# Kernel tuning notes

Hardware: AMD Instinct MI355X
Metric: run time of the kernel (lower is better)

The kernel has to match this reference:

```python
import jax, jax.numpy as jnp
import numpy as np

D = 512
B, S = 4, 4096


def setup_inputs() -> dict:
    key = jax.random.key(0)
    ks = jax.random.split(key, 8)
    scale = 1.0 / np.sqrt(D)
    return {
        "x": jax.random.normal(ks[0], (B, S, D), dtype=jnp.float32),
        "bias": jax.random.normal(ks[1], (1, S, S), dtype=jnp.float32),
        "Wq_w": jax.random.normal(ks[2], (D, D), dtype=jnp.float32) * scale,
        "Wq_b": jax.random.normal(ks[3], (D,), dtype=jnp.float32) * 0.02,
        "Wk_w": jax.random.normal(ks[4], (D, D), dtype=jnp.float32) * scale,
        "Wk_b": jax.random.normal(ks[5], (D,), dtype=jnp.float32) * 0.02,
        "Wv_w": jax.random.normal(ks[6], (D, D), dtype=jnp.float32) * scale,
        "Wv_b": jax.random.normal(ks[7], (D,), dtype=jnp.float32) * 0.02,
    }


def reference(x, bias, Wq_w, Wq_b, Wk_w, Wk_b, Wv_w, Wv_b):
    # torch nn.Linear: y = x @ W.T + b
    q = jnp.einsum("bsd,ed->bse", x, Wq_w) + Wq_b
    k = jnp.einsum("bsd,ed->bse", x, Wk_w) + Wk_b
    v = jnp.einsum("bsd,ed->bse", x, Wv_w) + Wv_b
    inv_sqrt_d = jnp.asarray(1.0 / np.sqrt(D), dtype=x.dtype)
    # scores: [B, S, S] -- scale by sqrt(feature_dim) as in the original
    scores = jnp.einsum("bqd,bkd->bqk", q * inv_sqrt_d, k) + bias
    weights = jax.nn.sigmoid(scores)
    out = jnp.einsum("bqk,bkd->bqd", weights, v)
    return out
```

## Files before the change

### kernel.cpp

```cpp
#include <hip/hip_runtime.h>
#include <hip/hip_bf16.h>
#include <stdint.h>

typedef unsigned short bf16_t;
typedef __attribute__((ext_vector_type(4))) short s4v;
typedef __attribute__((ext_vector_type(8))) short short8;
typedef __attribute__((ext_vector_type(4))) float f32x4;

__device__ __forceinline__ bf16_t f2b(float f) {
    union { float f; uint32_t u; } v; v.f = f;
    uint32_t u = v.u;
    return (bf16_t)((u + 0x7FFFu + ((u >> 16) & 1u)) >> 16);
}

__global__ __launch_bounds__(256) void cvt_all(const float* __restrict__ x,
                                               bf16_t* __restrict__ Xb,
                                               const float* __restrict__ a,
                                               const float* __restrict__ b,
                                               const float* __restrict__ c,
                                               bf16_t* __restrict__ Wb) {
    int i = blockIdx.x * 256 + threadIdx.x;
    if (i < 2097152) {
        float4 f = ((const float4*)x)[i];
        ushort4 o;
        o.x = f2b(f.x); o.y = f2b(f.y); o.z = f2b(f.z); o.w = f2b(f.w);
        ((ushort4*)Xb)[i] = o;
    } else {
        int j = i - 2097152;
        const int which = j >> 16;
        const int idx   = j & 65535;
        const float* src = (which == 0) ? a : (which == 1) ? b : c;
        float4 f = ((const float4*)src)[idx];
        ushort4 o;
        o.x = f2b(f.x); o.y = f2b(f.y); o.z = f2b(f.z); o.w = f2b(f.w);
        ((ushort4*)Wb)[j] = o;
    }
}

__device__ __forceinline__ void lds_dma16(const void* g, void* l) {
    __builtin_amdgcn_global_load_lds(
        (const __attribute__((address_space(1))) void*)g,
        (__attribute__((address_space(3))) void*)l, 16, 0, 0);
}


__global__ __launch_bounds__(256)
void proj_all(const bf16_t* __restrict__ Xb, const bf16_t* __restrict__ Wb,
              const float* __restrict__ qb, const float* __restrict__ kb,
              const float* __restrict__ vb,
              bf16_t* __restrict__ Qb, bf16_t* __restrict__ Kb,
              bf16_t* __restrict__ Vt)
{
    __shared__ __align__(16) bf16_t lds[2][16384];

    const int tid  = threadIdx.x;
    const int bid  = blockIdx.x;
    const int lane = tid & 63;
    const int w    = tid >> 6;
    const int wm   = w & 1, wn = w >> 1;
    const int ll   = lane & 15;
    const int quad = lane >> 4;

    const int x     = bid & 7;
    const int g     = bid >> 3;
    const int mi    = x * 16 + g / 12;
    const int inner = g % 12;
    const int m0 = mi * 128;
    const int n0 = (inner & 3) * 128;
    const int z  = inner >> 2;

    const bf16_t* A = Xb;
    const bf16_t* B = Wb + z * 262144;

    auto stage = [&](int kt, int b) {
#pragma unroll
        for (int c = 0; c < 4; ++c) {
            const int base = (c * 4 + w) * 64;
            const int slot = base + lane;
            const int row  = slot >> 3;
            const int kc   = ((slot & 7) ^ (row & 7)) << 3;
            lds_dma16(A + (size_t)(m0 + row) * 512 + kt * 64 + kc, (char*)&lds[b][0]    + base * 16);
            lds_dma16(B + (size_t)(n0 + row) * 512 + kt * 64 + kc, (char*)&lds[b][8192] + base * 16);
        }
    };

    f32x4 acc[4][4];
#pragma unroll
    for (int i = 0; i < 4; i++)
#pragma unroll
        for (int j = 0; j < 4; j++) acc[i][j] = (f32x4){0.f, 0.f, 0.f, 0.f};

    stage(0, 0);
    __syncthreads();
    int cur = 0;
    for (int kt = 0; kt < 8; ++kt) {
        if (kt < 7) stage(kt + 1, cur ^ 1);
        const bf16_t* lsA = &lds[cur][0];
        const bf16_t* lsB = &lds[cur][8192];
#pragma unroll
        for (int t = 0; t < 2; t++) {
            short8 af[4], bf[4];
#pragma unroll
            for (int i = 0; i < 4; i++) {
                const int ri = wm * 64 + i * 16 + ll;
                const int rj = wn * 64 + i * 16 + ll;
                af[i] = *(const short8*)(lsA + ri * 64 + (((t * 4 + quad) ^ (ll & 7)) << 3));
                bf[i] = *(const short8*)(lsB + rj * 64 + (((t * 4 + quad) ^ (ll & 7)) << 3));
            }
#pragma unroll
            for (int i = 0; i < 4; i++)
#pragma unroll
                for (int j = 0; j < 4; j++)
                    acc[i][j] = __builtin_amdgcn_mfma_f32_16x16x32_bf16(af[i], bf[j], acc[i][j], 0, 0, 0);
        }
        __syncthreads();
        cur ^= 1;
    }

    bf16_t* wbuf = &lds[0][0] + w * 4096;
    const float inv = 0.044194173824159216f;

    if (z != 2) {
        const float* bptr = (z == 0) ? qb : kb;
        const float scl   = (z == 0) ? inv : 1.0f;
#pragma unroll
        for (int j = 0; j < 4; j++) {
            const int colL = j * 16 + ll;
            const float bv = bptr[n0 + wn * 64 + colL];
#pragma unroll
            for (int i = 0; i < 4; i++) {
                f32x4 a = acc[i][j];
#pragma unroll
                for (int r = 0; r < 4; r++) {
                    const int rowL = i * 16 + quad * 4 + r;
                    wbuf[rowL * 64 + (colL ^ ((rowL & 7) << 3))] = f2b((a[r] + bv) * scl);
                }
            }
        }
        __syncthreads();
        bf16_t* dst = (z == 0) ? Qb : Kb;
        const int rowg0 = m0 + wm * 64;
        const int colg0 = n0 + wn * 64;
#pragma unroll
        for (int k = 0; k < 8; k++) {
            const int rowL = (lane >> 3) + k * 8;
            const int c0   = (lane & 7) * 8;
            short8 vv = *(const short8*)(wbuf + rowL * 64 + (c0 ^ ((rowL & 7) << 3)));
            *(short8*)(dst + (size_t)(rowg0 + rowL) * 512 + colg0 + c0) = vv;
        }
    } else {
#pragma unroll
        for (int j = 0; j < 4; j++) {
            const int d = j * 16 + ll;
            const float bv = vb[n0 + wn * 64 + d];
#pragma unroll
            for (int i = 0; i < 4; i++) {
                f32x4 a = acc[i][j];
                s4v pk;
                pk[0] = (short)f2b(a[0] + bv);
                pk[1] = (short)f2b(a[1] + bv);
                pk[2] = (short)f2b(a[2] + bv);
                pk[3] = (short)f2b(a[3] + bv);
                const int sB = i * 16 + quad * 4;
                *(s4v*)(wbuf + d * 64 + (sB ^ ((d & 7) << 3))) = pk;
            }
        }
        __syncthreads();
        const int rowg0 = m0 + wm * 64;
        const int b  = rowg0 >> 12;
        const int s0 = rowg0 & 4095;
        const int d0 = n0 + wn * 64;
#pragma unroll
        for (int k = 0; k < 8; k++) {
            const int dL = (lane >> 3) + k * 8;
            const int c0 = (lane & 7) * 8;
            short8 vv = *(const short8*)(wbuf + dL * 64 + (c0 ^ ((dL & 7) << 3)));
            *(short8*)(Vt + ((size_t)b * 512 + d0 + dL) * 4096 + s0 + c0) = vv;
        }
    }
}

__global__ __launch_bounds__(256)
void scores_sig(const bf16_t* __restrict__ Qb, const bf16_t* __restrict__ Kb,
                const float* __restrict__ bias, bf16_t* __restrict__ P)
{
    __shared__ __align__(16) bf16_t lds[2][16384];

    const int tid  = threadIdx.x;
    const int lane = tid & 63;
    const int w    = tid >> 6;
    const int wm   = w & 1, wn = w >> 1;
    const int ll   = lane & 15;
    const int quad = lane >> 4;

    const int bx  = blockIdx.x;
    const int x   = bx & 7;
    const int s   = bx >> 3;
    const int z   = s & 3;
    const int t_  = x * 128 + (s >> 2);
    const int sup = t_ >> 5;
    const int win = t_ & 31;
    const int m0  = ((sup >> 2) * 4 + (win & 3)) * 128;
    const int n0  = ((sup & 3) * 8 + (win >> 2)) * 128;

    const bf16_t* A = Qb + (size_t)z * 2097152;
    const bf16_t* B = Kb + (size_t)z * 2097152;
    bf16_t* out = P + (size_t)z * 16777216;

    auto stage = [&](int kt, int b) {
#pragma unroll
        for (int c = 0; c < 4; ++c) {
            const int base = (c * 4 + w) * 64;
            const int slot = base + lane;
            const int row  = slot >> 3;
            const int kc   = ((slot & 7) ^ (row & 7)) << 3;
            lds_dma16(A + (size_t)(m0 + row) * 512 + kt * 64 + kc, (char*)&lds[b][0]    + base * 16);
            lds_dma16(B + (size_t)(n0 + row) * 512 + kt * 64 + kc, (char*)&lds[b][8192] + base * 16);
        }
    };

    f32x4 acc[4][4];
#pragma unroll
    for (int i = 0; i < 4; i++)
#pragma unroll
        for (int j = 0; j < 4; j++) acc[i][j] = (f32x4){0.f, 0.f, 0.f, 0.f};

    stage(0, 0);
    __syncthreads();
    int cur = 0;
    for (int kt = 0; kt < 8; ++kt) {
        if (kt < 7) stage(kt + 1, cur ^ 1);
        const bf16_t* lsA = &lds[cur][0];
        const bf16_t* lsB = &lds[cur][8192];
#pragma unroll
        for (int t = 0; t < 2; t++) {
            short8 af[4], bf[4];
#pragma unroll
            for (int i = 0; i < 4; i++) {
                const int ri = wm * 64 + i * 16 + ll;
                const int rj = wn * 64 + i * 16 + ll;
                af[i] = *(const short8*)(lsA + ri * 64 + (((t * 4 + quad) ^ (ll & 7)) << 3));
                bf[i] = *(const short8*)(lsB + rj * 64 + (((t * 4 + quad) ^ (ll & 7)) << 3));
            }
#pragma unroll
            for (int i = 0; i < 4; i++)
#pragma unroll
                for (int j = 0; j < 4; j++)
                    acc[i][j] = __builtin_amdgcn_mfma_f32_16x16x32_bf16(af[i], bf[j], acc[i][j], 0, 0, 0);
        }
        __syncthreads();
        cur ^= 1;
    }

#pragma unroll
    for (int i = 0; i < 4; i++) {
#pragma unroll
        for (int j = 0; j < 4; j++) {
            const int col  = n0 + wn * 64 + j * 16 + ll;
            const int rowb = m0 + wm * 64 + i * 16 + quad * 4;
            f32x4 a = acc[i][j];
#pragma unroll
            for (int r = 0; r < 4; r++) {
                const int row = rowb + r;
                const float v = a[r] + bias[(size_t)row * 4096 + col];
                const float p = __builtin_amdgcn_rcpf(1.f + __expf(-v));
                out[(size_t)row * 4096 + col] = (bf16_t)(__float_as_uint(p) >> 16);
            }
        }
    }
}

__global__ __launch_bounds__(256)
void pv_gemm(const bf16_t* __restrict__ P, const bf16_t* __restrict__ Vt,
             float* __restrict__ outg)
{
    __shared__ __align__(16) bf16_t lds[2][16384];

    const int tid  = threadIdx.x;
    const int lane = tid & 63;
    const int w    = tid >> 6;
    const int wm   = w & 1, wn = w >> 1;
    const int ll   = lane & 15;
    const int quad = lane >> 4;

    const int bid   = blockIdx.x;
    const int x     = bid & 7;
    const int g     = bid >> 3;
    const int strip = x * 16 + (g >> 2);
    const int n0    = (g & 3) * 128;
    const int m0    = (strip & 31) * 128;
    const int z     = strip >> 5;

    const bf16_t* A = P + (size_t)z * 16777216;
    const bf16_t* B = Vt + (size_t)z * 2097152;
    float* out = outg + (size_t)z * 2097152;

    auto stage = [&](int kt, int b) {
#pragma unroll
        for (int c = 0; c < 4; ++c) {
            const int base = (c * 4 + w) * 64;
            const int slot = base + lane;
            const int row  = slot >> 3;
            const int kc   = ((slot & 7) ^ (row & 7)) << 3;
            lds_dma16(A + (size_t)(m0 + row) * 4096 + kt * 64 + kc, (char*)&lds[b][0]    + base * 16);
            lds_dma16(B + (size_t)(n0 + row) * 4096 + kt * 64 + kc, (char*)&lds[b][8192] + base * 16);
        }
    };

    f32x4 acc[4][4];
#pragma unroll
    for (int i = 0; i < 4; i++)
#pragma unroll
        for (int j = 0; j < 4; j++) acc[i][j] = (f32x4){0.f, 0.f, 0.f, 0.f};

    stage(0, 0);
    __syncthreads();
    int cur = 0;
    for (int kt = 0; kt < 64; ++kt) {
        if (kt < 63) stage(kt + 1, cur ^ 1);
        const bf16_t* lsA = &lds[cur][0];
        const bf16_t* lsB = &lds[cur][8192];
#pragma unroll
        for (int t = 0; t < 2; t++) {
            short8 af[4], bf[4];
#pragma unroll
            for (int i = 0; i < 4; i++) {
                const int ri = wm * 64 + i * 16 + ll;
                const int rj = wn * 64 + i * 16 + ll;
                af[i] = *(const short8*)(lsA + ri * 64 + (((t * 4 + quad) ^ (ll & 7)) << 3));
                bf[i] = *(const short8*)(lsB + rj * 64 + (((t * 4 + quad) ^ (ll & 7)) << 3));
            }
#pragma unroll
            for (int i = 0; i < 4; i++)
#pragma unroll
                for (int j = 0; j < 4; j++)
                    acc[i][j] = __builtin_amdgcn_mfma_f32_16x16x32_bf16(af[i], bf[j], acc[i][j], 0, 0, 0);
        }
        __syncthreads();
        cur ^= 1;
    }

#pragma unroll
    for (int i = 0; i < 4; i++) {
#pragma unroll
        for (int j = 0; j < 4; j++) {
            const int col  = n0 + wn * 64 + j * 16 + ll;
            const int rowb = m0 + wm * 64 + i * 16 + quad * 4;
            f32x4 a = acc[i][j];
#pragma unroll
            for (int r = 0; r < 4; r++)
                out[(size_t)(rowb + r) * 512 + col] = a[r];
        }
    }
}

extern "C" void kernel_launch(void* const* d_in, const int* in_sizes, int n_in,
                              void* d_out, int out_size, void* d_ws, size_t ws_size,
                              hipStream_t stream) {
    (void)in_sizes; (void)n_in; (void)out_size; (void)ws_size;
    const float* x    = (const float*)d_in[0];
    const float* bias = (const float*)d_in[1];
    const float* Wq_w = (const float*)d_in[2];
    const float* Wq_b = (const float*)d_in[3];
    const float* Wk_w = (const float*)d_in[4];
    const float* Wk_b = (const float*)d_in[5];
    const float* Wv_w = (const float*)d_in[6];
    const float* Wv_b = (const float*)d_in[7];
    float* out = (float*)d_out;

    bf16_t* Xb = (bf16_t*)d_ws;
    bf16_t* Wb = Xb + (size_t)16384 * 512;
    bf16_t* Qb = Wb + (size_t)3 * 512 * 512;
    bf16_t* Kb = Qb + (size_t)16384 * 512;
    bf16_t* Vt = Kb + (size_t)16384 * 512;
    bf16_t* P  = Vt + (size_t)16384 * 512;

    cvt_all<<<8960, 256, 0, stream>>>(x, Xb, Wq_w, Wk_w, Wv_w, Wb);

    proj_all<<<1536, 256, 0, stream>>>(Xb, Wb, Wq_b, Wk_b, Wv_b, Qb, Kb, Vt);
    scores_sig<<<4096, 256, 0, stream>>>(Qb, Kb, bias, P);
    pv_gemm<<<512, 256, 0, stream>>>(P, Vt, out);
}
```

Measured before the change: 366.7 us.

## Convert bias to bf16 inside projection kernel and reorder scores block mapping

The projection kernel now also converts the fp32 bias matrix into a bf16 copy, interleaved with its GEMM k-loop and written into the output buffer as scratch. The scores kernel then reads the bias as bf16, which halves its bias read traffic, and the batch index becomes the fastest-varying block index so the four batches sharing a bias tile run close together and can reuse it from cache. The cost is an extra full bias read and write during the projection kernel, plus bf16 rounding of the bias before the sigmoid. Using the output buffer as scratch depends on the final kernel overwriting it completely.

Result: no change. 363.3 us, median of 2 (-0.9%).

```diff
diff --git a/kernel.cpp b/kernel.cpp
--- a/kernel.cpp
+++ b/kernel.cpp
@@ -11,6 +11,12 @@
     union { float f; uint32_t u; } v; v.f = f;
     uint32_t u = v.u;
     return (bf16_t)((u + 0x7FFFu + ((u >> 16) & 1u)) >> 16);
+}
+
+__device__ __forceinline__ float b2f(bf16_t b) {
+    union { uint32_t u; float f; } v;
+    v.u = ((uint32_t)b) << 16;
+    return v.f;
 }
 
 __global__ __launch_bounds__(256) void cvt_all(const float* __restrict__ x,
@@ -49,7 +55,8 @@
               const float* __restrict__ qb, const float* __restrict__ kb,
               const float* __restrict__ vb,
               bf16_t* __restrict__ Qb, bf16_t* __restrict__ Kb,
-              bf16_t* __restrict__ Vt)
+              bf16_t* __restrict__ Vt,
+              const float* __restrict__ biasf, bf16_t* __restrict__ biasb)
 {
     __shared__ __align__(16) bf16_t lds[2][16384];
 
@@ -95,6 +102,22 @@
     int cur = 0;
     for (int kt = 0; kt < 8; ++kt) {
         if (kt < 7) stage(kt + 1, cur ^ 1);
+
+        {
+            const int idx = (bid * 8 + kt) * 256 + tid;
+            float4 f = ((const float4*)biasf)[idx];
+            ushort4 o;
+            o.x = f2b(f.x); o.y = f2b(f.y); o.z = f2b(f.z); o.w = f2b(f.w);
+            ((ushort4*)biasb)[idx] = o;
+            const int idx2 = idx + 3145728;
+            if (idx2 < 4194304) {
+                float4 f2 = ((const float4*)biasf)[idx2];
+                ushort4 o2;
+                o2.x = f2b(f2.x); o2.y = f2b(f2.y); o2.z = f2b(f2.z); o2.w = f2b(f2.w);
+                ((ushort4*)biasb)[idx2] = o2;
+            }
+        }
+
         const bf16_t* lsA = &lds[cur][0];
         const bf16_t* lsB = &lds[cur][8192];
 #pragma unroll
@@ -182,7 +205,7 @@
 
 __global__ __launch_bounds__(256)
 void scores_sig(const bf16_t* __restrict__ Qb, const bf16_t* __restrict__ Kb,
-                const float* __restrict__ bias, bf16_t* __restrict__ P)
+                const bf16_t* __restrict__ biasb, bf16_t* __restrict__ P)
 {
     __shared__ __align__(16) bf16_t lds[2][16384];
 
@@ -194,10 +217,8 @@
     const int quad = lane >> 4;
 
     const int bx  = blockIdx.x;
-    const int x   = bx & 7;
-    const int s   = bx >> 3;
-    const int z   = s & 3;
-    const int t_  = x * 128 + (s >> 2);
+    const int z   = bx & 3;
+    const int t_  = bx >> 2;
     const int sup = t_ >> 5;
     const int win = t_ & 31;
     const int m0  = ((sup >> 2) * 4 + (win & 3)) * 128;
@@ -262,7 +283,7 @@
 #pragma unroll
             for (int r = 0; r < 4; r++) {
                 const int row = rowb + r;
-                const float v = a[r] + bias[(size_t)row * 4096 + col];
+                const float v = a[r] + b2f(biasb[(size_t)row * 4096 + col]);
                 const float p = __builtin_amdgcn_rcpf(1.f + __expf(-v));
                 out[(size_t)row * 4096 + col] = (bf16_t)(__float_as_uint(p) >> 16);
             }
@@ -374,10 +395,12 @@
     bf16_t* Kb = Qb + (size_t)16384 * 512;
     bf16_t* Vt = Kb + (size_t)16384 * 512;
     bf16_t* P  = Vt + (size_t)16384 * 512;
+    bf16_t* Bb = (bf16_t*)d_out;
 
     cvt_all<<<8960, 256, 0, stream>>>(x, Xb, Wq_w, Wk_w, Wv_w, Wb);
 
-    proj_all<<<1536, 256, 0, stream>>>(Xb, Wb, Wq_b, Wk_b, Wv_b, Qb, Kb, Vt);
-    scores_sig<<<4096, 256, 0, stream>>>(Qb, Kb, bias, P);
+    proj_all<<<1536, 256, 0, stream>>>(Xb, Wb, Wq_b, Wk_b, Wv_b, Qb, Kb, Vt,
+                                       bias, Bb);
+    scores_sig<<<4096, 256, 0, stream>>>(Qb, Kb, Bb, P);
     pv_gemm<<<512, 256, 0, stream>>>(P, Vt, out);
 }
```
